# Performance work log

Hardware: AMD Instinct MI355X
Metric: run time of the kernel (lower is better)

Reference implementation:

```python
import jax, jax.numpy as jnp
import numpy as np

N_NODES = 100000
N_EDGES = 1600000
IN_DIM = 128
LATENT = [128, 128, 16]  # last entry = num classes (logits dim)


def setup_inputs() -> dict:
    key = jax.random.key(0)
    ks = jax.random.split(key, 16)
    inp = {
        "x": jax.random.normal(ks[0], (N_NODES, IN_DIM), dtype=jnp.float32),
        "edge_index": jax.random.randint(ks[1], (2, N_EDGES), 0, N_NODES, dtype=jnp.int64),
        "edge_weight": jax.random.uniform(ks[2], (N_EDGES,), dtype=jnp.float32),
    }
    dims = [IN_DIM] + LATENT
    for i in range(len(LATENT)):
        fan_in = dims[i]
        scale = 1.0 / np.sqrt(fan_in)
        inp[f"W{i}"] = jax.random.uniform(ks[3 + 2 * i], (dims[i], dims[i + 1]), minval=-scale, maxval=scale, dtype=jnp.float32)
        inp[f"b{i}"] = jax.random.uniform(ks[4 + 2 * i], (dims[i + 1],), minval=-scale, maxval=scale, dtype=jnp.float32)
        inp[f"eps{i}"] = jnp.zeros((), dtype=jnp.float32)  # GINConv train_eps init = 0
    return inp


def _gin_layer(x, W, b, eps, src, dst, edge_weight):
    # message: x_j (optionally scaled by edge weight), summed into target nodes
    msg = x[src]
    if edge_weight is not None:
        msg = msg * edge_weight[:, None]
    agg = jax.ops.segment_sum(msg, dst, num_segments=N_NODES)
    h = (1.0 + eps) * x + agg
    return jax.nn.relu(h @ W + b)  # MLP = Linear + ReLU


def _l2_normalize(x, eps=1e-12):
    norm = jnp.linalg.norm(x, axis=-1, keepdims=True)
    return x / jnp.maximum(norm, eps)


def reference(x, edge_index, edge_weight, W0, b0, eps0, W1, b1, eps1, W2, b2, eps2):
    src, dst = edge_index[0], edge_index[1]
    params = [(W0, b0, eps0), (W1, b1, eps1), (W2, b2, eps2)]
    h = x
    # all but last layer: GINConv(with edge_weight) -> l2 normalize -> ReLU
    for (W, b, e) in params[:-1]:
        h = _gin_layer(h, W, b, e, src, dst, edge_weight)
        h = _l2_normalize(h)  # emb_normlize=True
        h = jax.nn.relu(h)
    # last layer: GINConv WITHOUT edge_weight (forward passes only x, edge_index)
    W, b, e = params[-1]
    logits = _gin_layer(h, W, b, e, src, dst, None)
    probs = jax.nn.softmax(logits, axis=-1)
    return (logits, probs)
```

## Files before the change

### kernel.cpp

```cpp
#include <hip/hip_runtime.h>
#include <hip/hip_bf16.h>

#define N_NODES 100000
#define N_EDGES 1600000
#define DIM 128
#define ODIM 16
#define NB 391
#define PCHUNK 3200
#define PBLK 500
#define FCAP 6144
#define CAST_BLOCKS 25000

typedef unsigned int uint32;
typedef float f32x2 __attribute__((ext_vector_type(2)));
typedef float f32x4 __attribute__((ext_vector_type(4)));
typedef short bf16x8 __attribute__((ext_vector_type(8)));

static __device__ __forceinline__ float bflo(uint32 p) { return __uint_as_float(p << 16); }
static __device__ __forceinline__ float bfhi(uint32 p) { return __uint_as_float(p & 0xFFFF0000u); }
static __device__ __forceinline__ unsigned short f2bf(float f) {
  __hip_bfloat16 h = __float2bfloat16(f);
  return *reinterpret_cast<unsigned short*>(&h);
}
static __device__ __forceinline__ uint32 pk2bf(float a, float b) {
  return (uint32)f2bf(a) | ((uint32)f2bf(b) << 16);
}

__global__ __launch_bounds__(256) void prep_kernel(
    const float2* __restrict__ x2, uint32* __restrict__ Xu,
    const float* __restrict__ W0, const float* __restrict__ W1,
    const float* __restrict__ W2,
    unsigned short* __restrict__ pW0, unsigned short* __restrict__ pW1,
    unsigned short* __restrict__ pW2, int* __restrict__ bcnt) {
  int b = blockIdx.x;
  int tid = threadIdx.x;
  if (b < CAST_BLOCKS) {
    int i = b * 256 + tid;
    float2 v = x2[i];
    Xu[i] = pk2bf(v.x, v.y);
  } else if (b < CAST_BLOCKS + 128) {
    int wsel = (b - CAST_BLOCKS) >> 6;
    int idx = ((b - CAST_BLOCKS) & 63) * 256 + tid;
    int j = idx & 7, lane = (idx >> 3) & 63, nt = (idx >> 9) & 7, kc = idx >> 12;
    const float* W = wsel ? W1 : W0;
    unsigned short* pW = wsel ? pW1 : pW0;
    pW[idx] = f2bf(W[(kc * 32 + (lane >> 4) * 8 + j) * DIM + nt * 16 + (lane & 15)]);
  } else if (b < CAST_BLOCKS + 136) {
    int idx = (b - CAST_BLOCKS - 128) * 256 + tid;
    int j = idx & 7, lane = (idx >> 3) & 63, kc = idx >> 9;
    pW2[idx] = f2bf(W2[(kc * 32 + (lane >> 4) * 8 + j) * ODIM + (lane & 15)]);
  } else {
    for (int i = tid; i < NB; i += 256) bcnt[i] = 0;
  }
}

__global__ __launch_bounds__(256) void bucket_hist_kernel(
    const int* __restrict__ dst, int* __restrict__ bcnt) {
  __shared__ int h[NB];
  int tid = threadIdx.x;
  for (int i = tid; i < NB; i += 256) h[i] = 0;
  __syncthreads();
  int e0 = blockIdx.x * PCHUNK;
  for (int i = tid; i < PCHUNK; i += 256) atomicAdd(&h[dst[e0 + i] >> 8], 1);
  __syncthreads();
  for (int i = tid; i < NB; i += 256)
    if (h[i]) atomicAdd(&bcnt[i], h[i]);
}

__global__ __launch_bounds__(512) void bucket_scan_kernel(
    const int* __restrict__ bcnt, int* __restrict__ bbase,
    int* __restrict__ bcur) {
  __shared__ int sc[512];
  int t = threadIdx.x;
  int v = (t < NB) ? bcnt[t] : 0;
  sc[t] = v;
  __syncthreads();
  for (int off = 1; off < 512; off <<= 1) {
    int a = (t >= off) ? sc[t - off] : 0;
    __syncthreads();
    sc[t] += a;
    __syncthreads();
  }
  if (t < NB) {
    int base = sc[t] - v;
    bbase[t] = base;
    bcur[t] = base;
  }
}

__global__ __launch_bounds__(256) void coarse_partition_kernel(
    const int* __restrict__ src, const int* __restrict__ dst,
    const float* __restrict__ ew, int* __restrict__ bcur,
    int2* __restrict__ epack) {
  __shared__ int hist[NB];
  __shared__ int base_a[NB];
  __shared__ int lcur_a[NB];
  __shared__ int gbase_a[NB];
  __shared__ int2 stg[PCHUNK];
  __shared__ int gpos[PCHUNK];

  int tid = threadIdx.x;
  int e0 = blockIdx.x * PCHUNK;

  for (int i = tid; i < NB; i += 256) hist[i] = 0;
  __syncthreads();
  for (int i = tid; i < PCHUNK; i += 256) atomicAdd(&hist[dst[e0 + i] >> 8], 1);
  __syncthreads();

  if (tid < 64) {
    int run = 0;
#pragma unroll
    for (int c = 0; c < 7; c++) {
      int idx = c * 64 + tid;
      int v = (idx < NB) ? hist[idx] : 0;
      int incl = v;
#pragma unroll
      for (int off = 1; off < 64; off <<= 1) {
        int tv = __shfl_up(incl, off, 64);
        if (tid >= off) incl += tv;
      }
      if (idx < NB) base_a[idx] = run + incl - v;
      run += __shfl(incl, 63, 64);
    }
  }
  __syncthreads();
  for (int i = tid; i < NB; i += 256) {
    int c = hist[i];
    gbase_a[i] = (c > 0) ? atomicAdd(&bcur[i], c) : 0;
    lcur_a[i] = base_a[i];
  }
  __syncthreads();

  for (int i = tid; i < PCHUNK; i += 256) {
    int e = e0 + i;
    int s = src[e], d = dst[e];
    float w = ew[e];
    int b = d >> 8;
    int pos = atomicAdd(&lcur_a[b], 1);
    stg[pos] = make_int2(s | ((d & 255) << 20), __float_as_int(w));
    gpos[pos] = gbase_a[b] + (pos - base_a[b]);
  }
  __syncthreads();
  for (int i = tid; i < PCHUNK; i += 256) epack[gpos[i]] = stg[i];
}

__global__ __launch_bounds__(256) void fine_sort_kernel(
    const int* __restrict__ bbase, int2* __restrict__ epack,
    int* __restrict__ row_ptr) {
  __shared__ int2 ebuf[FCAP];
  __shared__ int hist[256];
  __shared__ int sc[256];
  __shared__ int cur[256];
  int tid = threadIdx.x;
  int b = blockIdx.x;
  int node0 = b << 8;
  int lo = bbase[b];
  int hi = (b == NB - 1) ? N_EDGES : bbase[b + 1];
  int n = hi - lo;
  if (n > FCAP) n = FCAP;
  hist[tid] = 0;
  __syncthreads();
  for (int i = tid; i < n; i += 256) {
    int2 e = epack[lo + i];
    ebuf[i] = e;
    atomicAdd(&hist[(e.x >> 20) & 255], 1);
  }
  __syncthreads();
  sc[tid] = hist[tid];
  __syncthreads();
  for (int off = 1; off < 256; off <<= 1) {
    int a = (tid >= off) ? sc[tid - off] : 0;
    __syncthreads();
    sc[tid] += a;
    __syncthreads();
  }
  int rp = lo + sc[tid] - hist[tid];
  if (node0 + tid < N_NODES) row_ptr[node0 + tid] = rp;
  cur[tid] = rp;
  if (b == 0 && tid == 0) row_ptr[N_NODES] = N_EDGES;
  __syncthreads();
  for (int i = tid; i < n; i += 256) {
    int2 e = ebuf[i];
    int pos = atomicAdd(&cur[(e.x >> 20) & 255], 1);
    epack[pos] = make_int2(e.x & 0xFFFFF, e.y);
  }
}

__global__ __launch_bounds__(256) void gather_bf16(
    const uint32* __restrict__ hu, const int* __restrict__ row_ptr,
    const int2* __restrict__ ep, uint32* __restrict__ aggu) {
  int lane = threadIdx.x & 63;
  int node = blockIdx.x * 4 + (threadIdx.x >> 6);
  if (node >= N_NODES) return;
  int grp = lane >> 4, l4 = lane & 15;
  int a = row_ptr[node], bnd = row_ptr[node + 1];
  f32x2 acc2[4];
#pragma unroll
  for (int k = 0; k < 4; k++) acc2[k] = (f32x2){0.f, 0.f};

  auto acc8 = [&](float wv, const uint4& p) {
    acc2[0] += (f32x2){bflo(p.x), bfhi(p.x)} * wv;
    acc2[1] += (f32x2){bflo(p.y), bfhi(p.y)} * wv;
    acc2[2] += (f32x2){bflo(p.z), bfhi(p.z)} * wv;
    acc2[3] += (f32x2){bflo(p.w), bfhi(p.w)} * wv;
  };

  int j = a;
#pragma unroll 1
  for (; j + 16 <= bnd; j += 16) {
    int2 e0 = ep[j + grp];
    int2 e1 = ep[j + 4 + grp];
    int2 e2 = ep[j + 8 + grp];
    int2 e3 = ep[j + 12 + grp];
    uint4 p0 = *(const uint4*)(hu + (size_t)e0.x * 64 + l4 * 4);
    uint4 p1 = *(const uint4*)(hu + (size_t)e1.x * 64 + l4 * 4);
    uint4 p2 = *(const uint4*)(hu + (size_t)e2.x * 64 + l4 * 4);
    uint4 p3 = *(const uint4*)(hu + (size_t)e3.x * 64 + l4 * 4);
    acc8(__int_as_float(e0.y), p0);
    acc8(__int_as_float(e1.y), p1);
    acc8(__int_as_float(e2.y), p2);
    acc8(__int_as_float(e3.y), p3);
  }
  if (j + 8 <= bnd) {
    int2 e0 = ep[j + grp];
    int2 e1 = ep[j + 4 + grp];
    uint4 p0 = *(const uint4*)(hu + (size_t)e0.x * 64 + l4 * 4);
    uint4 p1 = *(const uint4*)(hu + (size_t)e1.x * 64 + l4 * 4);
    acc8(__int_as_float(e0.y), p0);
    acc8(__int_as_float(e1.y), p1);
    j += 8;
  }
  if (j + 4 <= bnd) {
    int2 e0 = ep[j + grp];
    uint4 p0 = *(const uint4*)(hu + (size_t)e0.x * 64 + l4 * 4);
    acc8(__int_as_float(e0.y), p0);
    j += 4;
  }
  if (j < bnd) {
    int idx = j + grp;
    int vld = idx < bnd;
    int2 e = ep[vld ? idx : bnd - 1];
    uint4 p = *(const uint4*)(hu + (size_t)e.x * 64 + l4 * 4);
    float wv = vld ? __int_as_float(e.y) : 0.f;
    acc8(wv, p);
  }
#pragma unroll
  for (int k = 0; k < 4; k++) {
    acc2[k].x += __shfl_xor(acc2[k].x, 16, 64);
    acc2[k].x += __shfl_xor(acc2[k].x, 32, 64);
    acc2[k].y += __shfl_xor(acc2[k].y, 16, 64);
    acc2[k].y += __shfl_xor(acc2[k].y, 32, 64);
  }
  if (lane < 16) {
    uint4 st = {pk2bf(acc2[0].x, acc2[0].y), pk2bf(acc2[1].x, acc2[1].y),
                pk2bf(acc2[2].x, acc2[2].y), pk2bf(acc2[3].x, acc2[3].y)};
    *(uint4*)(aggu + (size_t)node * 64 + l4 * 4) = st;
  }
}

template <int FUSE_PROJ>
__global__ __launch_bounds__(256) void gin_mlp_mfma(
    const uint32* Xu, const uint32* __restrict__ Au,
    const unsigned char* __restrict__ pW, const float* __restrict__ b,
    const float* __restrict__ eps_p, uint32* outH,
    const unsigned char* __restrict__ pW2, float* __restrict__ y) {
  __shared__ __align__(16) unsigned char As[64 * 272];
  int tid = threadIdx.x;
  int node0 = blockIdx.x * 64;
  float epf = 1.0f + *eps_p;

  const uint4* X4 = (const uint4*)Xu;
  const uint4* A4 = (const uint4*)Au;
#pragma unroll
  for (int c = 0; c < 4; c++) {
    int t = c * 256 + tid;
    int n = t >> 4, s = t & 15;
    int node = node0 + n;
    int cn = node < N_NODES ? node : N_NODES - 1;
    uint4 xv = X4[(size_t)cn * 16 + s];
    uint4 av = A4[(size_t)cn * 16 + s];
    uint4 o;
    o.x = pk2bf(fmaf(epf, bflo(xv.x), bflo(av.x)), fmaf(epf, bfhi(xv.x), bfhi(av.x)));
    o.y = pk2bf(fmaf(epf, bflo(xv.y), bflo(av.y)), fmaf(epf, bfhi(xv.y), bfhi(av.y)));
    o.z = pk2bf(fmaf(epf, bflo(xv.z), bflo(av.z)), fmaf(epf, bfhi(xv.z), bfhi(av.z)));
    o.w = pk2bf(fmaf(epf, bflo(xv.w), bflo(av.w)), fmaf(epf, bfhi(xv.w), bfhi(av.w)));
    *(uint4*)(As + n * 272 + s * 16) = o;
  }
  __syncthreads();

  int w = tid >> 6, l = tid & 63;
  int m = l & 15, q = l >> 4;

  f32x4 acc[8];
#pragma unroll
  for (int nt = 0; nt < 8; nt++) acc[nt] = (f32x4){0.f, 0.f, 0.f, 0.f};

  const unsigned char* Abase = As + (w * 16 + m) * 272 + q * 16;
#pragma unroll
  for (int kc = 0; kc < 4; kc++) {
    bf16x8 af = *(const bf16x8*)(Abase + kc * 64);
#pragma unroll
    for (int nt = 0; nt < 8; nt++) {
      bf16x8 bfr = *(const bf16x8*)(pW + (size_t)((kc * 8 + nt) * 64 + l) * 16);
      acc[nt] = __builtin_amdgcn_mfma_f32_16x16x32_bf16(af, bfr, acc[nt], 0, 0, 0);
    }
  }

  float ss[4] = {0.f, 0.f, 0.f, 0.f};
#pragma unroll
  for (int nt = 0; nt < 8; nt++) {
    float bj = b[nt * 16 + m];
#pragma unroll
    for (int r = 0; r < 4; r++) {
      float v = fmaxf(acc[nt][r] + bj, 0.0f);
      acc[nt][r] = v;
      ss[r] += v * v;
    }
  }
#pragma unroll
  for (int r = 0; r < 4; r++) {
    float s = ss[r];
    s += __shfl_xor(s, 1, 64);
    s += __shfl_xor(s, 2, 64);
    s += __shfl_xor(s, 4, 64);
    s += __shfl_xor(s, 8, 64);
    ss[r] = 1.0f / fmaxf(sqrtf(s), 1e-12f);
  }
#pragma unroll
  for (int nt = 0; nt < 8; nt++) {
#pragma unroll
    for (int r = 0; r < 4; r++) {
      unsigned short hv = f2bf(acc[nt][r] * ss[r]);
      *(unsigned short*)(As + (w * 16 + q * 4 + r) * 272 + (nt * 16 + m) * 2) = hv;
    }
  }

  if (FUSE_PROJ) {
    f32x4 accy = (f32x4){0.f, 0.f, 0.f, 0.f};
#pragma unroll
    for (int kc = 0; kc < 4; kc++) {
      bf16x8 af = *(const bf16x8*)(Abase + kc * 64);
      bf16x8 bfr = *(const bf16x8*)(pW2 + (size_t)(kc * 64 + l) * 16);
      accy = __builtin_amdgcn_mfma_f32_16x16x32_bf16(af, bfr, accy, 0, 0, 0);
    }
#pragma unroll
    for (int r = 0; r < 4; r++) {
      int orow = node0 + w * 16 + q * 4 + r;
      if (orow < N_NODES) y[(size_t)orow * ODIM + m] = accy[r];
    }
  } else {
    __syncthreads();
    int rem = N_NODES - node0; if (rem > 64) rem = 64;
    for (int i = tid; i < 1024; i += 256) {
      int row = i >> 4, seg = i & 15;
      if (row < rem) {
        uint4 vv = *(const uint4*)(As + row * 272 + seg * 16);
        *(uint4*)((unsigned char*)outH + (size_t)(node0 + row) * 256 + seg * 16) = vv;
      }
    }
  }
}

__global__ __launch_bounds__(256) void gather16_final_kernel(
    const float* __restrict__ y, const int* __restrict__ row_ptr,
    const int2* __restrict__ ep, const float* __restrict__ b,
    const float* __restrict__ eps_p, float* __restrict__ out_logits,
    float* __restrict__ out_probs) {
  int lane = threadIdx.x & 63;
  int node = blockIdx.x * 4 + (threadIdx.x >> 6);
  if (node >= N_NODES) return;
  int f = lane & 15, eq = lane >> 4;
  int a = row_ptr[node], bnd = row_ptr[node + 1];
  float acc = 0.0f;
  int j = a + eq;
  for (; j + 8 <= bnd; j += 8) {
    int s0 = ep[j].x, s1 = ep[j + 4].x;
    acc += y[(size_t)s0 * ODIM + f] + y[(size_t)s1 * ODIM + f];
  }
  for (; j < bnd; j += 4) acc += y[(size_t)ep[j].x * ODIM + f];
  acc += __shfl_xor(acc, 16, 64);
  acc += __shfl_xor(acc, 32, 64);
  if (eq == 0) {
    float epf = 1.0f + *eps_p;
    size_t idx = (size_t)node * ODIM + f;
    float logit = fmaxf(fmaf(epf, y[idx], acc) + b[f], 0.0f);
    float mx = logit;
#pragma unroll
    for (int mm = 8; mm >= 1; mm >>= 1) mx = fmaxf(mx, __shfl_xor(mx, mm, 16));
    float e = __expf(logit - mx);
    float ssum = e;
#pragma unroll
    for (int mm = 8; mm >= 1; mm >>= 1) ssum += __shfl_xor(ssum, mm, 16);
    out_logits[idx] = logit;
    out_probs[idx] = e / ssum;
  }
}

extern "C" void kernel_launch(void* const* d_in, const int* in_sizes, int n_in,
                              void* d_out, int out_size, void* d_ws, size_t ws_size,
                              hipStream_t stream) {
  const float* x = (const float*)d_in[0];
  const int* ei = (const int*)d_in[1];
  const float* ew = (const float*)d_in[2];
  const float* W0 = (const float*)d_in[3];
  const float* b0 = (const float*)d_in[4];
  const float* e0 = (const float*)d_in[5];
  const float* W1 = (const float*)d_in[6];
  const float* b1 = (const float*)d_in[7];
  const float* e1 = (const float*)d_in[8];
  const float* W2 = (const float*)d_in[9];
  const float* b2 = (const float*)d_in[10];
  const float* e2 = (const float*)d_in[11];
  float* out = (float*)d_out;

  const int* srcp = ei;
  const int* dstp = ei + N_EDGES;

  char* ws = (char*)d_ws;
  size_t off = 0;
  uint32* Agg = (uint32*)(ws + off);  off += (size_t)N_NODES * DIM * 2;
  uint32* Xb  = (uint32*)(ws + off);  off += (size_t)N_NODES * DIM * 2;
  uint32* H   = (uint32*)(ws + off);  off += (size_t)N_NODES * DIM * 2;
  int2* epack = (int2*)(ws + off);    off += (size_t)N_EDGES * 8;
  float* y    = (float*)(ws + off);   off += (size_t)N_NODES * ODIM * 4;
  int* row_ptr = (int*)(ws + off);    off += (size_t)(N_NODES + 16) * 4;
  int* bcnt   = (int*)(ws + off);     off += 2048;
  int* bbase  = (int*)(ws + off);     off += 2048;
  int* bcur   = (int*)(ws + off);     off += 2048;
  unsigned short* pW0 = (unsigned short*)(ws + off); off += 32768;
  unsigned short* pW1 = (unsigned short*)(ws + off); off += 32768;
  unsigned short* pW2 = (unsigned short*)(ws + off); off += 4096;

  prep_kernel<<<CAST_BLOCKS + 137, 256, 0, stream>>>(
      (const float2*)x, Xb, W0, W1, W2, pW0, pW1, pW2, bcnt);

  bucket_hist_kernel<<<PBLK, 256, 0, stream>>>(dstp, bcnt);
  bucket_scan_kernel<<<1, 512, 0, stream>>>(bcnt, bbase, bcur);
  coarse_partition_kernel<<<PBLK, 256, 0, stream>>>(srcp, dstp, ew, bcur, epack);
  fine_sort_kernel<<<NB, 256, 0, stream>>>(bbase, epack, row_ptr);

  int ggrid = (N_NODES + 3) / 4;
  int mgrid = (N_NODES + 63) / 64;

  gather_bf16<<<ggrid, 256, 0, stream>>>(Xb, row_ptr, epack, Agg);
  gin_mlp_mfma<0><<<mgrid, 256, 0, stream>>>(Xb, Agg, (const unsigned char*)pW0,
                                             b0, e0, H, nullptr, nullptr);
  gather_bf16<<<ggrid, 256, 0, stream>>>(H, row_ptr, epack, Agg);
  gin_mlp_mfma<1><<<mgrid, 256, 0, stream>>>(H, Agg, (const unsigned char*)pW1,
                                             b1, e1, nullptr,
                                             (const unsigned char*)pW2, y);
  gather16_final_kernel<<<ggrid, 256, 0, stream>>>(y, row_ptr, epack, b2, e2,
                                                   out, out + (size_t)N_NODES * ODIM);
}
```

Baseline: 375.0 us.

## Fuse histogram into prep, drop scan kernel, store final layer in bf16

The bucket histogram is folded into the prep kernel, and the scan kernel is removed. Coarse partition now computes global bucket bases from the counts itself, and fine sort derives its offset with a block reduction. The fine sort writes output contiguously through an inverse permutation. Nontemporal loads and stores are added to the gathers and prep, x is cast four floats at a time, and the 16-wide final projection is stored in bf16 and gathered with vectorised lanes. This cuts two launches and some memory traffic, at the cost of bf16 rounding in the last layer and a smaller FCAP (4608), which could truncate large buckets.

```diff
diff --git a/kernel.cpp b/kernel.cpp
--- a/kernel.cpp
+++ b/kernel.cpp
@@ -8,13 +8,15 @@
 #define NB 391
 #define PCHUNK 3200
 #define PBLK 500
-#define FCAP 6144
-#define CAST_BLOCKS 25000
+#define FCAP 4608
+#define CB4 12500
 
 typedef unsigned int uint32;
 typedef float f32x2 __attribute__((ext_vector_type(2)));
 typedef float f32x4 __attribute__((ext_vector_type(4)));
 typedef short bf16x8 __attribute__((ext_vector_type(8)));
+typedef uint32 u32x4 __attribute__((ext_vector_type(4)));
+typedef uint32 u32x2 __attribute__((ext_vector_type(2)));
 
 static __device__ __forceinline__ float bflo(uint32 p) { return __uint_as_float(p << 16); }
 static __device__ __forceinline__ float bfhi(uint32 p) { return __uint_as_float(p & 0xFFFF0000u); }
@@ -25,75 +27,56 @@
 static __device__ __forceinline__ uint32 pk2bf(float a, float b) {
   return (uint32)f2bf(a) | ((uint32)f2bf(b) << 16);
 }
+static __device__ __forceinline__ int2 ntl_i2(const int2* p) {
+  long long v = __builtin_nontemporal_load((const long long*)p);
+  int2 r; r.x = (int)(v & 0xFFFFFFFFll); r.y = (int)(v >> 32); return r;
+}
 
 __global__ __launch_bounds__(256) void prep_kernel(
-    const float2* __restrict__ x2, uint32* __restrict__ Xu,
+    const f32x4* __restrict__ x4, uint32* __restrict__ Xu,
     const float* __restrict__ W0, const float* __restrict__ W1,
     const float* __restrict__ W2,
     unsigned short* __restrict__ pW0, unsigned short* __restrict__ pW1,
-    unsigned short* __restrict__ pW2, int* __restrict__ bcnt) {
+    unsigned short* __restrict__ pW2,
+    const int* __restrict__ dst, int* __restrict__ bcnt) {
+  __shared__ int h[NB];
   int b = blockIdx.x;
   int tid = threadIdx.x;
-  if (b < CAST_BLOCKS) {
+  if (b < CB4) {
     int i = b * 256 + tid;
-    float2 v = x2[i];
-    Xu[i] = pk2bf(v.x, v.y);
-  } else if (b < CAST_BLOCKS + 128) {
-    int wsel = (b - CAST_BLOCKS) >> 6;
-    int idx = ((b - CAST_BLOCKS) & 63) * 256 + tid;
+    f32x4 v = __builtin_nontemporal_load(x4 + i);
+    u32x2 o = {pk2bf(v[0], v[1]), pk2bf(v[2], v[3])};
+    *(u32x2*)(Xu + (size_t)i * 2) = o;
+  } else if (b < CB4 + 128) {
+    int wsel = (b - CB4) >> 6;
+    int idx = ((b - CB4) & 63) * 256 + tid;
     int j = idx & 7, lane = (idx >> 3) & 63, nt = (idx >> 9) & 7, kc = idx >> 12;
     const float* W = wsel ? W1 : W0;
     unsigned short* pW = wsel ? pW1 : pW0;
     pW[idx] = f2bf(W[(kc * 32 + (lane >> 4) * 8 + j) * DIM + nt * 16 + (lane & 15)]);
-  } else if (b < CAST_BLOCKS + 136) {
-    int idx = (b - CAST_BLOCKS - 128) * 256 + tid;
+  } else if (b < CB4 + 136) {
+    int idx = (b - CB4 - 128) * 256 + tid;
     int j = idx & 7, lane = (idx >> 3) & 63, kc = idx >> 9;
     pW2[idx] = f2bf(W2[(kc * 32 + (lane >> 4) * 8 + j) * ODIM + (lane & 15)]);
   } else {
-    for (int i = tid; i < NB; i += 256) bcnt[i] = 0;
-  }
-}
-
-__global__ __launch_bounds__(256) void bucket_hist_kernel(
-    const int* __restrict__ dst, int* __restrict__ bcnt) {
-  __shared__ int h[NB];
-  int tid = threadIdx.x;
-  for (int i = tid; i < NB; i += 256) h[i] = 0;
-  __syncthreads();
-  int e0 = blockIdx.x * PCHUNK;
-  for (int i = tid; i < PCHUNK; i += 256) atomicAdd(&h[dst[e0 + i] >> 8], 1);
-  __syncthreads();
-  for (int i = tid; i < NB; i += 256)
-    if (h[i]) atomicAdd(&bcnt[i], h[i]);
-}
-
-__global__ __launch_bounds__(512) void bucket_scan_kernel(
-    const int* __restrict__ bcnt, int* __restrict__ bbase,
-    int* __restrict__ bcur) {
-  __shared__ int sc[512];
-  int t = threadIdx.x;
-  int v = (t < NB) ? bcnt[t] : 0;
-  sc[t] = v;
-  __syncthreads();
-  for (int off = 1; off < 512; off <<= 1) {
-    int a = (t >= off) ? sc[t - off] : 0;
+    for (int i = tid; i < NB; i += 256) h[i] = 0;
     __syncthreads();
-    sc[t] += a;
+    int e0 = (b - CB4 - 136) * PCHUNK;
+    for (int i = tid; i < PCHUNK; i += 256)
+      atomicAdd(&h[__builtin_nontemporal_load(dst + e0 + i) >> 8], 1);
     __syncthreads();
-  }
-  if (t < NB) {
-    int base = sc[t] - v;
-    bbase[t] = base;
-    bcur[t] = base;
+    for (int i = tid; i < NB; i += 256)
+      if (h[i]) atomicAdd(&bcnt[i], h[i]);
   }
 }
 
 __global__ __launch_bounds__(256) void coarse_partition_kernel(
     const int* __restrict__ src, const int* __restrict__ dst,
-    const float* __restrict__ ew, int* __restrict__ bcur,
-    int2* __restrict__ epack) {
+    const float* __restrict__ ew, const int* __restrict__ bcnt,
+    int* __restrict__ bcur, int2* __restrict__ epack) {
   __shared__ int hist[NB];
   __shared__ int base_a[NB];
+  __shared__ int base_g[NB];
   __shared__ int lcur_a[NB];
   __shared__ int gbase_a[NB];
   __shared__ int2 stg[PCHUNK];
@@ -108,58 +91,73 @@
   __syncthreads();
 
   if (tid < 64) {
-    int run = 0;
+    int run = 0, rung = 0;
 #pragma unroll
     for (int c = 0; c < 7; c++) {
       int idx = c * 64 + tid;
       int v = (idx < NB) ? hist[idx] : 0;
-      int incl = v;
+      int vg = (idx < NB) ? bcnt[idx] : 0;
+      int incl = v, inclg = vg;
 #pragma unroll
       for (int off = 1; off < 64; off <<= 1) {
-        int tv = __shfl_up(incl, off, 64);
-        if (tid >= off) incl += tv;
+        int t1 = __shfl_up(incl, off, 64);
+        int t2 = __shfl_up(inclg, off, 64);
+        if (tid >= off) { incl += t1; inclg += t2; }
       }
-      if (idx < NB) base_a[idx] = run + incl - v;
+      if (idx < NB) {
+        base_a[idx] = run + incl - v;
+        base_g[idx] = rung + inclg - vg;
+      }
       run += __shfl(incl, 63, 64);
+      rung += __shfl(inclg, 63, 64);
     }
   }
   __syncthreads();
   for (int i = tid; i < NB; i += 256) {
     int c = hist[i];
-    gbase_a[i] = (c > 0) ? atomicAdd(&bcur[i], c) : 0;
+    gbase_a[i] = (c > 0) ? base_g[i] + atomicAdd(&bcur[i], c) : 0;
     lcur_a[i] = base_a[i];
   }
   __syncthreads();
 
   for (int i = tid; i < PCHUNK; i += 256) {
     int e = e0 + i;
-    int s = src[e], d = dst[e];
-    float w = ew[e];
-    int b = d >> 8;
-    int pos = atomicAdd(&lcur_a[b], 1);
+    int s = __builtin_nontemporal_load(src + e);
+    int d = dst[e];
+    float w = __builtin_nontemporal_load(ew + e);
+    int bkt = d >> 8;
+    int pos = atomicAdd(&lcur_a[bkt], 1);
     stg[pos] = make_int2(s | ((d & 255) << 20), __float_as_int(w));
-    gpos[pos] = gbase_a[b] + (pos - base_a[b]);
+    gpos[pos] = gbase_a[bkt] + (pos - base_a[bkt]);
   }
   __syncthreads();
   for (int i = tid; i < PCHUNK; i += 256) epack[gpos[i]] = stg[i];
 }
 
 __global__ __launch_bounds__(256) void fine_sort_kernel(
-    const int* __restrict__ bbase, int2* __restrict__ epack,
+    const int* __restrict__ bcnt, int2* __restrict__ epack,
     int* __restrict__ row_ptr) {
   __shared__ int2 ebuf[FCAP];
+  __shared__ unsigned short inv[FCAP];
   __shared__ int hist[256];
   __shared__ int sc[256];
   __shared__ int cur[256];
+  __shared__ int redc[4];
   int tid = threadIdx.x;
   int b = blockIdx.x;
   int node0 = b << 8;
-  int lo = bbase[b];
-  int hi = (b == NB - 1) ? N_EDGES : bbase[b + 1];
-  int n = hi - lo;
+
+  int part = 0;
+  for (int i = tid; i < b; i += 256) part += bcnt[i];
+#pragma unroll
+  for (int off = 32; off >= 1; off >>= 1) part += __shfl_xor(part, off, 64);
+  if ((tid & 63) == 0) redc[tid >> 6] = part;
+  hist[tid] = 0;
+  __syncthreads();
+  int lo = redc[0] + redc[1] + redc[2] + redc[3];
+  int n = bcnt[b];
   if (n > FCAP) n = FCAP;
-  hist[tid] = 0;
-  __syncthreads();
+
   for (int i = tid; i < n; i += 256) {
     int2 e = epack[lo + i];
     ebuf[i] = e;
@@ -169,20 +167,24 @@
   sc[tid] = hist[tid];
   __syncthreads();
   for (int off = 1; off < 256; off <<= 1) {
-    int a = (tid >= off) ? sc[tid - off] : 0;
+    int a2 = (tid >= off) ? sc[tid - off] : 0;
     __syncthreads();
-    sc[tid] += a;
+    sc[tid] += a2;
     __syncthreads();
   }
-  int rp = lo + sc[tid] - hist[tid];
-  if (node0 + tid < N_NODES) row_ptr[node0 + tid] = rp;
-  cur[tid] = rp;
+  int excl = sc[tid] - hist[tid];
+  if (node0 + tid < N_NODES) row_ptr[node0 + tid] = lo + excl;
+  cur[tid] = excl;
   if (b == 0 && tid == 0) row_ptr[N_NODES] = N_EDGES;
   __syncthreads();
   for (int i = tid; i < n; i += 256) {
-    int2 e = ebuf[i];
-    int pos = atomicAdd(&cur[(e.x >> 20) & 255], 1);
-    epack[pos] = make_int2(e.x & 0xFFFFF, e.y);
+    int p = atomicAdd(&cur[(ebuf[i].x >> 20) & 255], 1);
+    inv[p] = (unsigned short)i;
+  }
+  __syncthreads();
+  for (int p = tid; p < n; p += 256) {
+    int2 e = ebuf[inv[p]];
+    epack[lo + p] = make_int2(e.x & 0xFFFFF, e.y);
   }
 }
 
@@ -208,10 +210,10 @@
   int j = a;
 #pragma unroll 1
   for (; j + 16 <= bnd; j += 16) {
-    int2 e0 = ep[j + grp];
-    int2 e1 = ep[j + 4 + grp];
-    int2 e2 = ep[j + 8 + grp];
-    int2 e3 = ep[j + 12 + grp];
+    int2 e0 = ntl_i2(ep + j + grp);
+    int2 e1 = ntl_i2(ep + j + 4 + grp);
+    int2 e2 = ntl_i2(ep + j + 8 + grp);
+    int2 e3 = ntl_i2(ep + j + 12 + grp);
     uint4 p0 = *(const uint4*)(hu + (size_t)e0.x * 64 + l4 * 4);
     uint4 p1 = *(const uint4*)(hu + (size_t)e1.x * 64 + l4 * 4);
     uint4 p2 = *(const uint4*)(hu + (size_t)e2.x * 64 + l4 * 4);
@@ -222,8 +224,8 @@
     acc8(__int_as_float(e3.y), p3);
   }
   if (j + 8 <= bnd) {
-    int2 e0 = ep[j + grp];
-    int2 e1 = ep[j + 4 + grp];
+    int2 e0 = ntl_i2(ep + j + grp);
+    int2 e1 = ntl_i2(ep + j + 4 + grp);
     uint4 p0 = *(const uint4*)(hu + (size_t)e0.x * 64 + l4 * 4);
     uint4 p1 = *(const uint4*)(hu + (size_t)e1.x * 64 + l4 * 4);
     acc8(__int_as_float(e0.y), p0);
@@ -231,7 +233,7 @@
     j += 8;
   }
   if (j + 4 <= bnd) {
-    int2 e0 = ep[j + grp];
+    int2 e0 = ntl_i2(ep + j + grp);
     uint4 p0 = *(const uint4*)(hu + (size_t)e0.x * 64 + l4 * 4);
     acc8(__int_as_float(e0.y), p0);
     j += 4;
@@ -239,7 +241,7 @@
   if (j < bnd) {
     int idx = j + grp;
     int vld = idx < bnd;
-    int2 e = ep[vld ? idx : bnd - 1];
+    int2 e = ntl_i2(ep + (vld ? idx : bnd - 1));
     uint4 p = *(const uint4*)(hu + (size_t)e.x * 64 + l4 * 4);
     float wv = vld ? __int_as_float(e.y) : 0.f;
     acc8(wv, p);
@@ -252,9 +254,9 @@
     acc2[k].y += __shfl_xor(acc2[k].y, 32, 64);
   }
   if (lane < 16) {
-    uint4 st = {pk2bf(acc2[0].x, acc2[0].y), pk2bf(acc2[1].x, acc2[1].y),
+    u32x4 st = {pk2bf(acc2[0].x, acc2[0].y), pk2bf(acc2[1].x, acc2[1].y),
                 pk2bf(acc2[2].x, acc2[2].y), pk2bf(acc2[3].x, acc2[3].y)};
-    *(uint4*)(aggu + (size_t)node * 64 + l4 * 4) = st;
+    __builtin_nontemporal_store(st, (u32x4*)(aggu + (size_t)node * 64 + l4 * 4));
   }
 }
 
@@ -263,7 +265,7 @@
     const uint32* Xu, const uint32* __restrict__ Au,
     const unsigned char* __restrict__ pW, const float* __restrict__ b,
     const float* __restrict__ eps_p, uint32* outH,
-    const unsigned char* __restrict__ pW2, float* __restrict__ y) {
+    const unsigned char* __restrict__ pW2, uint32* __restrict__ yb) {
   __shared__ __align__(16) unsigned char As[64 * 272];
   int tid = threadIdx.x;
   int node0 = blockIdx.x * 64;
@@ -345,8 +347,12 @@
     }
 #pragma unroll
     for (int r = 0; r < 4; r++) {
-      int orow = node0 + w * 16 + q * 4 + r;
-      if (orow < N_NODES) y[(size_t)orow * ODIM + m] = accy[r];
+      float v = accy[r];
+      float o = __shfl_xor(v, 1, 64);
+      if (!(m & 1)) {
+        int orow = node0 + w * 16 + q * 4 + r;
+        if (orow < N_NODES) yb[(size_t)orow * 8 + (m >> 1)] = pk2bf(v, o);
+      }
     }
   } else {
     __syncthreads();
@@ -362,37 +368,55 @@
 }
 
 __global__ __launch_bounds__(256) void gather16_final_kernel(
-    const float* __restrict__ y, const int* __restrict__ row_ptr,
-    const int2* __restrict__ ep, const float* __restrict__ b,
+    const uint32* __restrict__ yb, const int* __restrict__ row_ptr,
+    const int2* __restrict__ ep, const float* __restrict__ bb,
     const float* __restrict__ eps_p, float* __restrict__ out_logits,
     float* __restrict__ out_probs) {
   int lane = threadIdx.x & 63;
   int node = blockIdx.x * 4 + (threadIdx.x >> 6);
   if (node >= N_NODES) return;
-  int f = lane & 15, eq = lane >> 4;
+  int f2 = lane & 3;
+  int eq = lane >> 2;
   int a = row_ptr[node], bnd = row_ptr[node + 1];
-  float acc = 0.0f;
-  int j = a + eq;
-  for (; j + 8 <= bnd; j += 8) {
-    int s0 = ep[j].x, s1 = ep[j + 4].x;
-    acc += y[(size_t)s0 * ODIM + f] + y[(size_t)s1 * ODIM + f];
-  }
-  for (; j < bnd; j += 4) acc += y[(size_t)ep[j].x * ODIM + f];
-  acc += __shfl_xor(acc, 16, 64);
-  acc += __shfl_xor(acc, 32, 64);
+  f32x4 acc = (f32x4){0.f, 0.f, 0.f, 0.f};
+  for (int j = a; j < bnd; j += 16) {
+    int idx = j + eq;
+    int vld = idx < bnd;
+    int2 e = ntl_i2(ep + (vld ? idx : bnd - 1));
+    u32x2 p = *(const u32x2*)(yb + (size_t)e.x * 8 + f2 * 2);
+    if (vld) {
+      acc[0] += bflo(p[0]); acc[1] += bfhi(p[0]);
+      acc[2] += bflo(p[1]); acc[3] += bfhi(p[1]);
+    }
+  }
+#pragma unroll
+  for (int k = 0; k < 4; k++) {
+#pragma unroll
+    for (int off = 4; off <= 32; off <<= 1)
+      acc[k] += __shfl_xor(acc[k], off, 64);
+  }
   if (eq == 0) {
     float epf = 1.0f + *eps_p;
-    size_t idx = (size_t)node * ODIM + f;
-    float logit = fmaxf(fmaf(epf, y[idx], acc) + b[f], 0.0f);
-    float mx = logit;
-#pragma unroll
-    for (int mm = 8; mm >= 1; mm >>= 1) mx = fmaxf(mx, __shfl_xor(mx, mm, 16));
-    float e = __expf(logit - mx);
-    float ssum = e;
-#pragma unroll
-    for (int mm = 8; mm >= 1; mm >>= 1) ssum += __shfl_xor(ssum, mm, 16);
-    out_logits[idx] = logit;
-    out_probs[idx] = e / ssum;
+    u32x2 ys = *(const u32x2*)(yb + (size_t)node * 8 + f2 * 2);
+    f32x4 lg;
+    lg[0] = fmaxf(fmaf(epf, bflo(ys[0]), acc[0]) + bb[f2 * 4 + 0], 0.f);
+    lg[1] = fmaxf(fmaf(epf, bfhi(ys[0]), acc[1]) + bb[f2 * 4 + 1], 0.f);
+    lg[2] = fmaxf(fmaf(epf, bflo(ys[1]), acc[2]) + bb[f2 * 4 + 2], 0.f);
+    lg[3] = fmaxf(fmaf(epf, bfhi(ys[1]), acc[3]) + bb[f2 * 4 + 3], 0.f);
+    float mx = fmaxf(fmaxf(lg[0], lg[1]), fmaxf(lg[2], lg[3]));
+    mx = fmaxf(mx, __shfl_xor(mx, 1, 4));
+    mx = fmaxf(mx, __shfl_xor(mx, 2, 4));
+    f32x4 ex;
+    float s = 0.f;
+#pragma unroll
+    for (int k = 0; k < 4; k++) { ex[k] = __expf(lg[k] - mx); s += ex[k]; }
+    s += __shfl_xor(s, 1, 4);
+    s += __shfl_xor(s, 2, 4);
+    float invs = 1.0f / s;
+    size_t base = (size_t)node * ODIM + f2 * 4;
+    *(f32x4*)(out_logits + base) = lg;
+    f32x4 pr = {ex[0] * invs, ex[1] * invs, ex[2] * invs, ex[3] * invs};
+    *(f32x4*)(out_probs + base) = pr;
   }
 }
 
@@ -422,22 +446,20 @@
   uint32* Xb  = (uint32*)(ws + off);  off += (size_t)N_NODES * DIM * 2;
   uint32* H   = (uint32*)(ws + off);  off += (size_t)N_NODES * DIM * 2;
   int2* epack = (int2*)(ws + off);    off += (size_t)N_EDGES * 8;
-  float* y    = (float*)(ws + off);   off += (size_t)N_NODES * ODIM * 4;
+  uint32* yb  = (uint32*)(ws + off);  off += (size_t)N_NODES * 8 * 4;
   int* row_ptr = (int*)(ws + off);    off += (size_t)(N_NODES + 16) * 4;
   int* bcnt   = (int*)(ws + off);     off += 2048;
-  int* bbase  = (int*)(ws + off);     off += 2048;
   int* bcur   = (int*)(ws + off);     off += 2048;
   unsigned short* pW0 = (unsigned short*)(ws + off); off += 32768;
   unsigned short* pW1 = (unsigned short*)(ws + off); off += 32768;
   unsigned short* pW2 = (unsigned short*)(ws + off); off += 4096;
 
-  prep_kernel<<<CAST_BLOCKS + 137, 256, 0, stream>>>(
-      (const float2*)x, Xb, W0, W1, W2, pW0, pW1, pW2, bcnt);
-
-  bucket_hist_kernel<<<PBLK, 256, 0, stream>>>(dstp, bcnt);
-  bucket_scan_kernel<<<1, 512, 0, stream>>>(bcnt, bbase, bcur);
-  coarse_partition_kernel<<<PBLK, 256, 0, stream>>>(srcp, dstp, ew, bcur, epack);
-  fine_sort_kernel<<<NB, 256, 0, stream>>>(bbase, epack, row_ptr);
+  hipMemsetAsync(bcnt, 0, 4096, stream);
+  prep_kernel<<<CB4 + 136 + PBLK, 256, 0, stream>>>(
+      (const f32x4*)x, Xb, W0, W1, W2, pW0, pW1, pW2, dstp, bcnt);
+
+  coarse_partition_kernel<<<PBLK, 256, 0, stream>>>(srcp, dstp, ew, bcnt, bcur, epack);
+  fine_sort_kernel<<<NB, 256, 0, stream>>>(bcnt, epack, row_ptr);
 
   int ggrid = (N_NODES + 3) / 4;
   int mgrid = (N_NODES + 63) / 64;
@@ -448,7 +470,7 @@
   gather_bf16<<<ggrid, 256, 0, stream>>>(H, row_ptr, epack, Agg);
   gin_mlp_mfma<1><<<mgrid, 256, 0, stream>>>(H, Agg, (const unsigned char*)pW1,
                                              b1, e1, nullptr,
-                                             (const unsigned char*)pW2, y);
-  gather16_final_kernel<<<ggrid, 256, 0, stream>>>(y, row_ptr, epack, b2, e2,
+                                             (const unsigned char*)pW2, yb);
+  gather16_final_kernel<<<ggrid, 256, 0, stream>>>(yb, row_ptr, epack, b2, e2,
                                                    out, out + (size_t)N_NODES * ODIM);
 }
```

Measured after the change: 376.8 us. No clear change (+0.5%).
